# Optimization experiments

Measured on AMD Instinct MI355X. Metric: run time of the kernel, lower is better.

Reference implementation:

```python
import jax, jax.numpy as jnp
import numpy as np

NEG_SLOPE = 0.2
N_NODES = 50000
N_EDGES = 800000
IN_DIM = 256
HID_DIM = 256
HEADS = 8
HEAD_DIM = HID_DIM // HEADS


def setup_inputs() -> dict:
    key = jax.random.key(0)
    ks = jax.random.split(key, 12)
    def glorot(k, shape):
        fan = sum(shape[-2:]) if len(shape) > 1 else shape[-1] + 1
        return jax.random.normal(k, shape, jnp.float32) * jnp.sqrt(2.0 / fan)
    return {
        "data": jax.random.normal(ks[0], (N_NODES, IN_DIM), jnp.float32),
        "src": jax.random.randint(ks[1], (N_EDGES,), 0, N_NODES),
        "dst": jax.random.randint(ks[2], (N_EDGES,), 0, N_NODES),
        "W1": glorot(ks[3], (IN_DIM, HID_DIM)),
        "al1": glorot(ks[4], (HEADS, HEAD_DIM)),
        "ar1": glorot(ks[5], (HEADS, HEAD_DIM)),
        "b1": jnp.zeros((HID_DIM,), jnp.float32),
        "W2": glorot(ks[6], (HID_DIM, HID_DIM)),
        "al2": glorot(ks[7], (HEADS, HEAD_DIM)),
        "ar2": glorot(ks[8], (HEADS, HEAD_DIM)),
        "b2": jnp.zeros((HID_DIM,), jnp.float32),
    }


def gat_layer(x, src, dst, W, al, ar, b):
    """One DGL-style GATConv layer with ReLU activation."""
    N = x.shape[0]
    feat = (x @ W).reshape(N, HEADS, HEAD_DIM)            # [N,H,D]
    el = jnp.sum(feat * al[None], axis=-1)                # [N,H]
    er = jnp.sum(feat * ar[None], axis=-1)                # [N,H]
    e = el[src] + er[dst]                                  # [E,H]
    e = jnp.where(e > 0, e, NEG_SLOPE * e)                 # LeakyReLU(0.2)
    # segment softmax over incoming edges of each dst node
    m = jax.ops.segment_max(e, dst, num_segments=N)        # [N,H] (-inf for empty)
    a = jnp.exp(e - m[dst])                                # [E,H]
    denom = jax.ops.segment_sum(a, dst, num_segments=N)    # [N,H]
    alpha = a / denom[dst]                                 # [E,H]
    msg = feat[src] * alpha[:, :, None]                    # [E,H,D]
    out = jax.ops.segment_sum(msg, dst, num_segments=N)    # [N,H,D]
    out = out + b.reshape(1, HEADS, HEAD_DIM)
    out = jax.nn.relu(out)
    return out.reshape(N, HID_DIM)


def reference(data, src, dst, W1, al1, ar1, b1, W2, al2, ar2, b2):
    h = gat_layer(data, src, dst, W1, al1, ar1, b1)
    h = gat_layer(h, src, dst, W2, al2, ar2, b2)
    return h
```

## Files before the change

### kernel.cpp

```cpp
#include <hip/hip_runtime.h>

#define N_NODES 50000
#define N_EDGES 800000
#define DIM 256
#define HEADS 8
#define NEG_SLOPE 0.2f
#define MAXDEG 64
#define OVFCAP 65536

typedef unsigned short u16;
typedef float floatx4 __attribute__((ext_vector_type(4)));
typedef __bf16 bf16x8 __attribute__((ext_vector_type(8)));

__device__ __forceinline__ float b2f(u16 u) {
    union { unsigned int i; float f; } v; v.i = ((unsigned int)u) << 16; return v.f;
}
__device__ __forceinline__ u16 f2b(float f) {
    union { float f; unsigned int i; } v; v.f = f;
    unsigned int x = v.i;
    if ((x & 0x7f800000u) == 0x7f800000u && (x & 0x007fffffu)) {
        return (u16)((x >> 16) | 0x0040u);
    }
    unsigned int r = (x + 0x7fffu + ((x >> 16) & 1u)) >> 16;
    return (u16)r;
}

__global__ __launch_bounds__(256) void fill_u32(unsigned int* __restrict__ p,
                                                unsigned int v, int n) {
    int i = blockIdx.x * 256 + threadIdx.x;
    if (i < n) p[i] = v;
}

__global__ __launch_bounds__(256) void init_kernel(const unsigned int* __restrict__ d,
                                                   int* __restrict__ counts,
                                                   int* __restrict__ flag,
                                                   int* __restrict__ novf) {
    int i = blockIdx.x * 256 + threadIdx.x;
    if (i < N_NODES) counts[i] = 0;
    if (blockIdx.x == 0) {
        __shared__ int cnt;
        if (threadIdx.x == 0) { cnt = 0; *novf = 0; }
        __syncthreads();
        unsigned int w = d[threadIdx.x];
        int bad = 0;
        #pragma unroll
        for (int half = 0; half < 2; ++half) {
            u16 u = (u16)(w >> (16 * half));
            unsigned int e = (u >> 7) & 0xFFu;
            if (u != 0 && (e >= 141u || e <= 27u)) bad = 1;
        }
        atomicAdd(&cnt, bad);
        __syncthreads();
        if (threadIdx.x == 0) *flag = (cnt > 64) ? 1 : 0;
    }
}

__global__ __launch_bounds__(256) void prep_kernel(const void* __restrict__ W1,
                                                   const void* __restrict__ W2,
                                                   u16* __restrict__ Wt1,
                                                   u16* __restrict__ Wt2,
                                                   const int* __restrict__ flagp) {
    const int isf = *flagp;
    int b = blockIdx.x;
    const void* W = (b < 16) ? W1 : W2;
    u16* Wt = (b < 16) ? Wt1 : Wt2;
    int t = b & 15;
    int k0 = (t >> 2) * 64, n0 = (t & 3) * 64;
    __shared__ float lt[64][65];
    int c = threadIdx.x & 63, r0 = threadIdx.x >> 6;
    #pragma unroll
    for (int j = 0; j < 16; ++j) {
        int r = j * 4 + r0;
        lt[r][c] = isf ? ((const float*)W)[(k0 + r) * 256 + n0 + c]
                       : b2f(((const u16*)W)[(k0 + r) * 256 + n0 + c]);
    }
    __syncthreads();
    #pragma unroll
    for (int j = 0; j < 16; ++j) {
        int rn = j * 4 + r0;
        Wt[(n0 + rn) * 256 + k0 + c] = f2b(lt[c][rn]);
    }
}

__global__ __launch_bounds__(256) void build_kernel(const int* __restrict__ src,
                                                    const int* __restrict__ dst,
                                                    int* __restrict__ counts,
                                                    int* __restrict__ padded,
                                                    int* __restrict__ novf,
                                                    int2* __restrict__ ovf, int E) {
    int i = blockIdx.x * 256 + threadIdx.x;
    if (i < E) {
        int d = dst[i];
        int s = src[i];
        int pos = atomicAdd(&counts[d], 1);
        if (pos < MAXDEG) {
            padded[d * MAXDEG + pos] = s;
        } else {
            int oi = atomicAdd(novf, 1);
            if (oi < OVFCAP) { int2 pr; pr.x = d; pr.y = s; ovf[oi] = pr; }
        }
    }
}

__global__ __launch_bounds__(256) void hist_kernel(const int* __restrict__ dst,
                                                   int* __restrict__ counts, int E) {
    int i = blockIdx.x * 256 + threadIdx.x;
    if (i < E) atomicAdd(&counts[dst[i]], 1);
}

__global__ __launch_bounds__(256) void scan_partial(const int* __restrict__ counts,
                                                    int* __restrict__ partial, int n) {
    int b = blockIdx.x, tid = threadIdx.x;
    int base = b * 1024 + tid * 4;
    int s = 0;
    #pragma unroll
    for (int k = 0; k < 4; ++k) if (base + k < n) s += counts[base + k];
    int lane = tid & 63;
    #pragma unroll
    for (int off = 32; off; off >>= 1) s += __shfl_xor(s, off);
    __shared__ int wsum[4];
    if (lane == 0) wsum[tid >> 6] = s;
    __syncthreads();
    if (tid == 0) partial[b] = wsum[0] + wsum[1] + wsum[2] + wsum[3];
}

__global__ __launch_bounds__(64) void scan_offsets(const int* __restrict__ partial,
                                                   int* __restrict__ offsets,
                                                   int* __restrict__ row_ptr,
                                                   int nb, int n) {
    int t = threadIdx.x;
    int v0 = (t < nb) ? partial[t] : 0;
    int v = v0;
    #pragma unroll
    for (int d = 1; d < 64; d <<= 1) {
        int u = __shfl_up(v, d);
        if (t >= d) v += u;
    }
    if (t < nb) offsets[t] = v - v0;
    if (t == 63) row_ptr[n] = v;
}

__global__ __launch_bounds__(256) void scan_write(const int* __restrict__ counts,
                                                  const int* __restrict__ offsets,
                                                  int* __restrict__ row_ptr,
                                                  int* __restrict__ wptr, int n) {
    int b = blockIdx.x, tid = threadIdx.x;
    int base = b * 1024 + tid * 4;
    int v[4]; int s = 0;
    #pragma unroll
    for (int k = 0; k < 4; ++k) { v[k] = (base + k < n) ? counts[base + k] : 0; s += v[k]; }
    int lane = tid & 63, w = tid >> 6;
    int incl = s;
    #pragma unroll
    for (int d = 1; d < 64; d <<= 1) {
        int u = __shfl_up(incl, d);
        if (lane >= d) incl += u;
    }
    __shared__ int wsum[4];
    if (lane == 63) wsum[w] = incl;
    __syncthreads();
    int woff = 0;
    for (int i = 0; i < w; ++i) woff += wsum[i];
    int run = offsets[b] + woff + incl - s;
    #pragma unroll
    for (int k = 0; k < 4; ++k) {
        if (base + k < n) { row_ptr[base + k] = run; wptr[base + k] = run; run += v[k]; }
    }
}

__global__ __launch_bounds__(256) void scatter_kernel(const int* __restrict__ src,
                                                      const int* __restrict__ dst,
                                                      int* __restrict__ wptr,
                                                      int* __restrict__ src_sorted, int E) {
    int i = blockIdx.x * 256 + threadIdx.x;
    if (i < E) {
        int pos = atomicAdd(&wptr[dst[i]], 1);
        src_sorted[pos] = src[i];
    }
}

#define LDA 264

__global__ __launch_bounds__(256, 3) void gemm_fused(const void* __restrict__ Araw,
                                                     int maybe_f32,
                                                     const u16* __restrict__ Wt,
                                                     u16* __restrict__ outF,
                                                     float* __restrict__ el,
                                                     float* __restrict__ er,
                                                     const void* __restrict__ al,
                                                     const void* __restrict__ ar,
                                                     int M, const int* __restrict__ flagp) {
    const int isf = *flagp;
    const bool af32 = (maybe_f32 != 0) && (isf != 0);
    __shared__ u16 As[64][LDA];
    const int tid  = threadIdx.x;
    const int w    = tid >> 6;
    const int lane = tid & 63;
    const int quad = lane >> 4;
    const int l16  = lane & 15;
    const int m0   = blockIdx.x * 64;

    const u16* wbase = Wt + (size_t)(64 * w + l16) * 256 + quad * 8;

    bf16x8 bCur[4], bNxt[4], aCur[4], aNxt[4];
    #pragma unroll
    for (int t = 0; t < 4; ++t)
        bCur[t] = *(const bf16x8*)(wbase + (size_t)t * 16 * 256);

    if (af32) {
        const float* Af = (const float*)Araw;
        #pragma unroll
        for (int it = 0; it < 8; ++it) {
            int idx = it * 256 + tid;
            int r = idx >> 5;
            int c = (idx & 31) << 3;
            int gr = m0 + r;
            u16 tb[8];
            if (gr < M) {
                float4 f0 = *(const float4*)(Af + (size_t)gr * 256 + c);
                float4 f1 = *(const float4*)(Af + (size_t)gr * 256 + c + 4);
                tb[0] = f2b(f0.x); tb[1] = f2b(f0.y); tb[2] = f2b(f0.z); tb[3] = f2b(f0.w);
                tb[4] = f2b(f1.x); tb[5] = f2b(f1.y); tb[6] = f2b(f1.z); tb[7] = f2b(f1.w);
            } else {
                #pragma unroll
                for (int k = 0; k < 8; ++k) tb[k] = 0;
            }
            *(uint4*)&As[r][c] = *(uint4*)tb;
        }
    } else {
        const u16* Ab = (const u16*)Araw;
        #pragma unroll
        for (int it = 0; it < 8; ++it) {
            int idx = it * 256 + tid;
            int r = idx >> 5;
            int c = (idx & 31) << 3;
            int gr = m0 + r;
            if (gr < M) {
                *(uint4*)&As[r][c] = *(const uint4*)(Ab + (size_t)gr * 256 + c);
            } else {
                uint4 z = {0u, 0u, 0u, 0u};
                *(uint4*)&As[r][c] = z;
            }
        }
    }
    __syncthreads();

    #pragma unroll
    for (int i = 0; i < 4; ++i)
        aCur[i] = *(const bf16x8*)&As[16 * i + l16][quad * 8];

    floatx4 acc[4][4] = {};

    #pragma unroll
    for (int s = 0; s < 8; ++s) {
        if (s < 7) {
            #pragma unroll
            for (int t = 0; t < 4; ++t)
                bNxt[t] = *(const bf16x8*)(wbase + (size_t)t * 16 * 256 + (s + 1) * 32);
            #pragma unroll
            for (int i = 0; i < 4; ++i)
                aNxt[i] = *(const bf16x8*)&As[16 * i + l16][(s + 1) * 32 + quad * 8];
        }
        #pragma unroll
        for (int i = 0; i < 4; ++i)
            #pragma unroll
            for (int t = 0; t < 4; ++t)
                acc[i][t] = __builtin_amdgcn_mfma_f32_16x16x32_bf16(aCur[i], bCur[t], acc[i][t], 0, 0, 0);
        if (s < 7) {
            #pragma unroll
            for (int t = 0; t < 4; ++t) bCur[t] = bNxt[t];
            #pragma unroll
            for (int i = 0; i < 4; ++i) aCur[i] = aNxt[i];
        }
    }

    __syncthreads();
    u16* Ct = (u16*)As;
    #pragma unroll
    for (int i = 0; i < 4; ++i)
        #pragma unroll
        for (int t = 0; t < 4; ++t) {
            int col = 64 * w + 16 * t + l16;
            #pragma unroll
            for (int r = 0; r < 4; ++r)
                Ct[(16 * i + quad * 4 + r) * LDA + col] = f2b(acc[i][t][r]);
        }
    __syncthreads();
    #pragma unroll
    for (int it = 0; it < 4; ++it) {
        int idx = it * 256 + tid;
        int row = idx >> 4;
        int c16 = (idx & 15) * 16;
        int gr = m0 + row;
        if (gr < M) {
            uint4 v0 = *(const uint4*)&Ct[row * LDA + c16];
            uint4 v1 = *(const uint4*)&Ct[row * LDA + c16 + 8];
            *(uint4*)(outF + (size_t)gr * 256 + c16) = v0;
            *(uint4*)(outF + (size_t)gr * 256 + c16 + 8) = v1;
        }
    }

    float alv[4], arv[4];
    #pragma unroll
    for (int t = 0; t < 4; ++t) {
        int c = 64 * w + 16 * t + l16;
        alv[t] = isf ? ((const float*)al)[c] : b2f(((const u16*)al)[c]);
        arv[t] = isf ? ((const float*)ar)[c] : b2f(((const u16*)ar)[c]);
    }
    #pragma unroll
    for (int i = 0; i < 4; ++i)
        #pragma unroll
        for (int r = 0; r < 4; ++r) {
            int row = m0 + 16 * i + quad * 4 + r;
            #pragma unroll
            for (int tt = 0; tt < 2; ++tt) {
                float pl = acc[i][2 * tt][r] * alv[2 * tt] + acc[i][2 * tt + 1][r] * alv[2 * tt + 1];
                float pr = acc[i][2 * tt][r] * arv[2 * tt] + acc[i][2 * tt + 1][r] * arv[2 * tt + 1];
                #pragma unroll
                for (int mask = 1; mask <= 8; mask <<= 1) {
                    pl += __shfl_xor(pl, mask);
                    pr += __shfl_xor(pr, mask);
                }
                if (l16 == 0 && row < M) {
                    el[row * 8 + 2 * w + tt] = pl;
                    er[row * 8 + 2 * w + tt] = pr;
                }
            }
        }
}

__global__ __launch_bounds__(256) void aggregate_kernel(const u16* __restrict__ feat,
                                                        const float* __restrict__ el,
                                                        const float* __restrict__ er,
                                                        const void* __restrict__ bias,
                                                        const int* __restrict__ idxinfo,
                                                        const int* __restrict__ srcbuf,
                                                        void* __restrict__ out,
                                                        int out_mode,
                                                        int node0,
                                                        const int* __restrict__ flagp,
                                                        int pmode,
                                                        const int* __restrict__ novfp,
                                                        const int2* __restrict__ ovf) {
    const int isf = *flagp;
    const int lane = threadIdx.x & 63;
    const int node = node0 + blockIdx.x * 4 + (threadIdx.x >> 6);
    if (node >= N_NODES) return;
    const int h = lane >> 3;
    const int j = lane & 7;
    int beg, deg;
    if (pmode) { beg = node * MAXDEG; deg = idxinfo[node]; }
    else       { beg = idxinfo[node]; deg = idxinfo[node + 1] - beg; }
    const int dcap = (pmode && deg > MAXDEG) ? MAXDEG : deg;
    int nov = 0;
    if (pmode && deg > MAXDEG) { nov = *novfp; if (nov > OVFCAP) nov = OVFCAP; }
    const float ern = er[node * HEADS + h];

    float m0v = -1e30f, ss0 = 0.f;
    float m1v = -1e30f, ss1 = 0.f;
    for (int i = j; i < dcap; i += 16) {
        int s0 = srcbuf[beg + i];
        int i2 = i + 8;
        int s1 = (i2 < dcap) ? srcbuf[beg + i2] : 0;
        float e0 = el[s0 * 8 + h] + ern;
        float e1 = el[s1 * 8 + h] + ern;
        e0 = e0 > 0.f ? e0 : NEG_SLOPE * e0;
        e1 = e1 > 0.f ? e1 : NEG_SLOPE * e1;
        if (i2 >= dcap) e1 = -3e30f;
        float mn0 = fmaxf(m0v, e0);
        ss0 = ss0 * __expf(m0v - mn0) + __expf(e0 - mn0);
        m0v = mn0;
        float mn1 = fmaxf(m1v, e1);
        ss1 = ss1 * __expf(m1v - mn1) + __expf(e1 - mn1);
        m1v = mn1;
    }
    for (int k = j; k < nov; k += 8) {
        int2 pr = ovf[k];
        if (pr.x != node) continue;
        float e = el[pr.y * 8 + h] + ern;
        e = e > 0.f ? e : NEG_SLOPE * e;
        float mn = fmaxf(m0v, e);
        ss0 = ss0 * __expf(m0v - mn) + __expf(e - mn);
        m0v = mn;
    }
    float m = fmaxf(m0v, m1v);
    float ssum = ss0 * __expf(m0v - m) + ss1 * __expf(m1v - m);
    #pragma unroll
    for (int mask = 1; mask <= 4; mask <<= 1) {
        float mo = __shfl_xor(m, mask);
        float so = __shfl_xor(ssum, mask);
        float mn = fmaxf(m, mo);
        ssum = ssum * __expf(m - mn) + so * __expf(mo - mn);
        m = mn;
    }
    const float mx = m;
    const float inv = ssum > 0.f ? 1.f / ssum : 0.f;

    const int q = lane & 31;
    const int half = lane >> 5;
    const int hq = q >> 2;
    float a[8] = {};

    int sC = 0; float avC = 0.f;
    if (j < dcap) {
        sC = srcbuf[beg + j];
        float e = el[sC * 8 + h] + ern;
        e = e > 0.f ? e : NEG_SLOPE * e;
        avC = __expf(e - mx) * inv;
    }
    uint4 f[4]; float ae[4];
    #pragma unroll
    for (int u = 0; u < 4; ++u) {
        int sel = hq * 8 + 2 * u + half;
        int se = __shfl(sC, sel);
        ae[u] = __shfl(avC, sel);
        f[u] = *(const uint4*)(feat + (size_t)se * DIM + 8 * q);
    }

    #pragma unroll 2
    for (int c0 = 0; c0 < dcap; c0 += 8) {
        uint4 f2[4]; float ae2[4];
        {
            int sN = 0; float avN = 0.f;
            int i = c0 + 8 + j;
            if (i < dcap) {
                sN = srcbuf[beg + i];
                float e = el[sN * 8 + h] + ern;
                e = e > 0.f ? e : NEG_SLOPE * e;
                avN = __expf(e - mx) * inv;
            }
            #pragma unroll
            for (int u = 0; u < 4; ++u) {
                int sel = hq * 8 + 2 * u + half;
                int se = __shfl(sN, sel);
                ae2[u] = __shfl(avN, sel);
                f2[u] = *(const uint4*)(feat + (size_t)se * DIM + 8 * q);
            }
        }
        #pragma unroll
        for (int u = 0; u < 4; ++u) {
            float wgt = ae[u];
            a[0] += wgt * b2f((u16)(f[u].x & 0xffffu)); a[1] += wgt * b2f((u16)(f[u].x >> 16));
            a[2] += wgt * b2f((u16)(f[u].y & 0xffffu)); a[3] += wgt * b2f((u16)(f[u].y >> 16));
            a[4] += wgt * b2f((u16)(f[u].z & 0xffffu)); a[5] += wgt * b2f((u16)(f[u].z >> 16));
            a[6] += wgt * b2f((u16)(f[u].w & 0xffffu)); a[7] += wgt * b2f((u16)(f[u].w >> 16));
        }
        #pragma unroll
        for (int u = 0; u < 4; ++u) { f[u] = f2[u]; ae[u] = ae2[u]; }
    }

    if (nov) {
        const float mxq  = __shfl(mx, hq * 8);
        const float invq = __shfl(inv, hq * 8);
        const float ernq = __shfl(ern, hq * 8);
        for (int k = 0; k < nov; ++k) {
            int2 pr = ovf[k];
            if (pr.x != node) continue;
            float av = 0.f;
            if (half == 0) {
                float e = el[pr.y * 8 + hq] + ernq;
                e = e > 0.f ? e : NEG_SLOPE * e;
                av = __expf(e - mxq) * invq;
            }
            uint4 fv = *(const uint4*)(feat + (size_t)pr.y * DIM + 8 * q);
            a[0] += av * b2f((u16)(fv.x & 0xffffu)); a[1] += av * b2f((u16)(fv.x >> 16));
            a[2] += av * b2f((u16)(fv.y & 0xffffu)); a[3] += av * b2f((u16)(fv.y >> 16));
            a[4] += av * b2f((u16)(fv.z & 0xffffu)); a[5] += av * b2f((u16)(fv.z >> 16));
            a[6] += av * b2f((u16)(fv.w & 0xffffu)); a[7] += av * b2f((u16)(fv.w >> 16));
        }
    }

    #pragma unroll
    for (int k = 0; k < 8; ++k) a[k] += __shfl_xor(a[k], 32);

    if (half == 0) {
        float o[8];
        if (isf) {
            float4 b0 = *(const float4*)((const float*)bias + 8 * q);
            float4 b1 = *(const float4*)((const float*)bias + 8 * q + 4);
            o[0] = a[0] + b0.x; o[1] = a[1] + b0.y; o[2] = a[2] + b0.z; o[3] = a[3] + b0.w;
            o[4] = a[4] + b1.x; o[5] = a[5] + b1.y; o[6] = a[6] + b1.z; o[7] = a[7] + b1.w;
        } else {
            uint4 bu = *(const uint4*)((const u16*)bias + 8 * q);
            o[0] = a[0] + b2f((u16)(bu.x & 0xffffu)); o[1] = a[1] + b2f((u16)(bu.x >> 16));
            o[2] = a[2] + b2f((u16)(bu.y & 0xffffu)); o[3] = a[3] + b2f((u16)(bu.y >> 16));
            o[4] = a[4] + b2f((u16)(bu.z & 0xffffu)); o[5] = a[5] + b2f((u16)(bu.z >> 16));
            o[6] = a[6] + b2f((u16)(bu.w & 0xffffu)); o[7] = a[7] + b2f((u16)(bu.w >> 16));
        }
        #pragma unroll
        for (int k = 0; k < 8; ++k) o[k] = fmaxf(o[k], 0.f);
        if (out_mode == 0 || !isf) {
            u16 pk[8] = {f2b(o[0]), f2b(o[1]), f2b(o[2]), f2b(o[3]),
                         f2b(o[4]), f2b(o[5]), f2b(o[6]), f2b(o[7])};
            *(uint4*)((u16*)out + (size_t)node * DIM + 8 * q) = *(uint4*)pk;
        } else {
            float4 v0 = {o[0], o[1], o[2], o[3]};
            float4 v1 = {o[4], o[5], o[6], o[7]};
            *(float4*)((float*)out + (size_t)node * DIM + 8 * q) = v0;
            *(float4*)((float*)out + (size_t)node * DIM + 8 * q + 4) = v1;
        }
    }
}

extern "C" void kernel_launch(void* const* d_in, const int* in_sizes, int n_in,
                              void* d_out, int out_size, void* d_ws, size_t ws_size,
                              hipStream_t stream) {
    const void* data = d_in[0];
    const int* src = (const int*)d_in[1];
    const int* dst = (const int*)d_in[2];
    const void* W1  = d_in[3];
    const void* al1 = d_in[4];
    const void* ar1 = d_in[5];
    const void* b1  = d_in[6];
    const void* W2  = d_in[7];
    const void* al2 = d_in[8];
    const void* ar2 = d_in[9];
    const void* b2  = d_in[10];

    const size_t BASE =
        (size_t)N_NODES * DIM * 2 +
        (size_t)N_NODES * HEADS * 4 * 2 +
        (size_t)N_NODES * 4 +
        2 * 256 * 256 * 2 +
        1024;
    const size_t NEEDED_PAD = BASE + (size_t)N_NODES * MAXDEG * 4 + (size_t)OVFCAP * 8;
    const size_t NEEDED_CSR = BASE + (size_t)N_NODES * 4 +
                              (size_t)(N_NODES + 4) * 4 +
                              (size_t)N_EDGES * 4;

    if (ws_size < NEEDED_CSR && ws_size < NEEDED_PAD) {
        int nwords = (out_size + 1) / 2;
        fill_u32<<<(nwords + 255) / 256, 256, 0, stream>>>(
            (unsigned int*)d_out, 0x42C842C8u, nwords);
        return;
    }

    char* ws = (char*)d_ws;
    u16* feat = (u16*)ws;        ws += (size_t)N_NODES * DIM * 2;
    float* el = (float*)ws;      ws += (size_t)N_NODES * HEADS * 4;
    float* er = (float*)ws;      ws += (size_t)N_NODES * HEADS * 4;
    int* counts = (int*)ws;      ws += (size_t)N_NODES * 4;
    u16* Wt1 = (u16*)ws;         ws += 256 * 256 * 2;
    u16* Wt2 = (u16*)ws;         ws += 256 * 256 * 2;
    int* flag = (int*)ws;        ws += 256;
    int* novf = (int*)ws;        ws += 256;
    int* partial = (int*)ws;     ws += 256;
    int* offsets = (int*)ws;     ws += 256;

    u16* h1 = (u16*)d_out;
    const int gemm_blocks = (N_NODES + 63) / 64;
    const int HALF = 25000;
    const int agg_half_blocks = HALF / 4;

    init_kernel<<<(N_NODES + 255) / 256, 256, 0, stream>>>(
        (const unsigned int*)data, counts, flag, novf);
    prep_kernel<<<32, 256, 0, stream>>>(W1, W2, Wt1, Wt2, flag);

    const int* idxinfo;
    const int* srcbuf;
    const int2* ovf = (const int2*)d_ws;
    int pmode;

    if (ws_size >= NEEDED_PAD) {
        int* padded = (int*)ws;  ws += (size_t)N_NODES * MAXDEG * 4;
        int2* ovfw = (int2*)ws;  ws += (size_t)OVFCAP * 8;
        build_kernel<<<(N_EDGES + 255) / 256, 256, 0, stream>>>(
            src, dst, counts, padded, novf, ovfw, N_EDGES);
        idxinfo = counts; srcbuf = padded; ovf = ovfw; pmode = 1;
    } else {
        int* wptr = (int*)ws;        ws += (size_t)N_NODES * 4;
        int* row_ptr = (int*)ws;     ws += (size_t)(N_NODES + 4) * 4;
        int* src_sorted = (int*)ws;  ws += (size_t)N_EDGES * 4;
        const int nb = (N_NODES + 1023) / 1024;
        hist_kernel<<<(N_EDGES + 255) / 256, 256, 0, stream>>>(dst, counts, N_EDGES);
        scan_partial<<<nb, 256, 0, stream>>>(counts, partial, N_NODES);
        scan_offsets<<<1, 64, 0, stream>>>(partial, offsets, row_ptr, nb, N_NODES);
        scan_write<<<nb, 256, 0, stream>>>(counts, offsets, row_ptr, wptr, N_NODES);
        scatter_kernel<<<(N_EDGES + 255) / 256, 256, 0, stream>>>(src, dst, wptr, src_sorted, N_EDGES);
        idxinfo = row_ptr; srcbuf = src_sorted; pmode = 0;
    }

    gemm_fused<<<gemm_blocks, 256, 0, stream>>>(data, 1, Wt1, feat,
                                                el, er, al1, ar1, N_NODES, flag);
    aggregate_kernel<<<agg_half_blocks, 256, 0, stream>>>(feat, el, er, b1, idxinfo, srcbuf,
                                                          (void*)h1, 0, 0, flag, pmode, novf, ovf);
    aggregate_kernel<<<agg_half_blocks, 256, 0, stream>>>(feat, el, er, b1, idxinfo, srcbuf,
                                                          (void*)h1, 0, HALF, flag, pmode, novf, ovf);
    gemm_fused<<<gemm_blocks, 256, 0, stream>>>(h1, 0, Wt2, feat,
                                                el, er, al2, ar2, N_NODES, flag);
    aggregate_kernel<<<agg_half_blocks, 256, 0, stream>>>(feat, el, er, b2, idxinfo, srcbuf,
                                                          d_out, 2, 0, flag, pmode, novf, ovf);
    aggregate_kernel<<<agg_half_blocks, 256, 0, stream>>>(feat, el, er, b2, idxinfo, srcbuf,
                                                          d_out, 2, HALF, flag, pmode, novf, ovf);
}
```

Before: 394.4 us.

## Fuse edge-list build into first GEMM launch and shrink GEMM tile to 32 rows

Merges the padded adjacency build kernel with the first-layer GEMM into one launch, interleaving build blocks and GEMM blocks 1:2 so the atomic-heavy build overlaps the MFMA work. The GEMM drops the LDS staging of A and of the output: A fragments are loaded straight from global into registers, and results are written directly to global memory. The tile is halved to 32 rows with occupancy 4. This removes a launch and the LDS traffic, but adds uncoalesced 2-byte output stores and redundant A loads across the four waves.

```diff
diff --git a/kernel.cpp b/kernel.cpp
--- a/kernel.cpp
+++ b/kernel.cpp
@@ -82,26 +82,6 @@
     }
 }
 
-__global__ __launch_bounds__(256) void build_kernel(const int* __restrict__ src,
-                                                    const int* __restrict__ dst,
-                                                    int* __restrict__ counts,
-                                                    int* __restrict__ padded,
-                                                    int* __restrict__ novf,
-                                                    int2* __restrict__ ovf, int E) {
-    int i = blockIdx.x * 256 + threadIdx.x;
-    if (i < E) {
-        int d = dst[i];
-        int s = src[i];
-        int pos = atomicAdd(&counts[d], 1);
-        if (pos < MAXDEG) {
-            padded[d * MAXDEG + pos] = s;
-        } else {
-            int oi = atomicAdd(novf, 1);
-            if (oi < OVFCAP) { int2 pr; pr.x = d; pr.y = s; ovf[oi] = pr; }
-        }
-    }
-}
-
 __global__ __launch_bounds__(256) void hist_kernel(const int* __restrict__ dst,
                                                    int* __restrict__ counts, int E) {
     int i = blockIdx.x * 256 + threadIdx.x;
@@ -179,126 +159,86 @@
     }
 }
 
-#define LDA 264
-
-__global__ __launch_bounds__(256, 3) void gemm_fused(const void* __restrict__ Araw,
-                                                     int maybe_f32,
-                                                     const u16* __restrict__ Wt,
-                                                     u16* __restrict__ outF,
-                                                     float* __restrict__ el,
-                                                     float* __restrict__ er,
-                                                     const void* __restrict__ al,
-                                                     const void* __restrict__ ar,
-                                                     int M, const int* __restrict__ flagp) {
-    const int isf = *flagp;
+__device__ __forceinline__ void gemm_body(int gid, const void* __restrict__ Araw,
+                                          int maybe_f32,
+                                          const u16* __restrict__ Wt,
+                                          u16* __restrict__ outF,
+                                          float* __restrict__ el,
+                                          float* __restrict__ er,
+                                          const void* __restrict__ al,
+                                          const void* __restrict__ ar,
+                                          int M, int isf) {
     const bool af32 = (maybe_f32 != 0) && (isf != 0);
-    __shared__ u16 As[64][LDA];
     const int tid  = threadIdx.x;
     const int w    = tid >> 6;
     const int lane = tid & 63;
     const int quad = lane >> 4;
     const int l16  = lane & 15;
-    const int m0   = blockIdx.x * 64;
+    const int m0   = gid * 32;
 
     const u16* wbase = Wt + (size_t)(64 * w + l16) * 256 + quad * 8;
-
-    bf16x8 bCur[4], bNxt[4], aCur[4], aNxt[4];
-    #pragma unroll
-    for (int t = 0; t < 4; ++t)
-        bCur[t] = *(const bf16x8*)(wbase + (size_t)t * 16 * 256);
-
-    if (af32) {
-        const float* Af = (const float*)Araw;
+    const float* Af = (const float*)Araw;
+    const u16* Ab = (const u16*)Araw;
+    const int rbase = m0 + l16;
+
+    u16 zb[8] = {};
+    const bf16x8 ZERO = *(const bf16x8*)zb;
+
+    bf16x8 aC[2], aN[2], bC[4], bN[4];
+    floatx4 acc[2][4] = {};
+
+#define LOADB(s, dstb) { \
+    _Pragma("unroll") \
+    for (int t = 0; t < 4; ++t) \
+        dstb[t] = *(const bf16x8*)(wbase + (size_t)t * 16 * 256 + (s) * 32); }
+
+#define LOADA(s, dsta) { \
+    _Pragma("unroll") \
+    for (int i = 0; i < 2; ++i) { \
+        int row_ = rbase + 16 * i; \
+        if (row_ < M) { \
+            if (af32) { \
+                const float* p_ = Af + (size_t)row_ * 256 + (s) * 32 + quad * 8; \
+                float4 f0_ = *(const float4*)p_; \
+                float4 f1_ = *(const float4*)(p_ + 4); \
+                u16 tb_[8] = {f2b(f0_.x), f2b(f0_.y), f2b(f0_.z), f2b(f0_.w), \
+                              f2b(f1_.x), f2b(f1_.y), f2b(f1_.z), f2b(f1_.w)}; \
+                dsta[i] = *(const bf16x8*)tb_; \
+            } else { \
+                dsta[i] = *(const bf16x8*)(Ab + (size_t)row_ * 256 + (s) * 32 + quad * 8); \
+            } \
+        } else dsta[i] = ZERO; } }
+
+    LOADB(0, bC);
+    LOADA(0, aC);
+
+    #pragma unroll
+    for (int s = 0; s < 8; ++s) {
+        if (s < 7) { LOADB(s + 1, bN); LOADA(s + 1, aN); }
         #pragma unroll
-        for (int it = 0; it < 8; ++it) {
-            int idx = it * 256 + tid;
-            int r = idx >> 5;
-            int c = (idx & 31) << 3;
-            int gr = m0 + r;
-            u16 tb[8];
-            if (gr < M) {
-                float4 f0 = *(const float4*)(Af + (size_t)gr * 256 + c);
-                float4 f1 = *(const float4*)(Af + (size_t)gr * 256 + c + 4);
-                tb[0] = f2b(f0.x); tb[1] = f2b(f0.y); tb[2] = f2b(f0.z); tb[3] = f2b(f0.w);
-                tb[4] = f2b(f1.x); tb[5] = f2b(f1.y); tb[6] = f2b(f1.z); tb[7] = f2b(f1.w);
-            } else {
-                #pragma unroll
-                for (int k = 0; k < 8; ++k) tb[k] = 0;
-            }
-            *(uint4*)&As[r][c] = *(uint4*)tb;
-        }
-    } else {
-        const u16* Ab = (const u16*)Araw;
-        #pragma unroll
-        for (int it = 0; it < 8; ++it) {
-            int idx = it * 256 + tid;
-            int r = idx >> 5;
-            int c = (idx & 31) << 3;
-            int gr = m0 + r;
-            if (gr < M) {
-                *(uint4*)&As[r][c] = *(const uint4*)(Ab + (size_t)gr * 256 + c);
-            } else {
-                uint4 z = {0u, 0u, 0u, 0u};
-                *(uint4*)&As[r][c] = z;
-            }
-        }
-    }
-    __syncthreads();
-
-    #pragma unroll
-    for (int i = 0; i < 4; ++i)
-        aCur[i] = *(const bf16x8*)&As[16 * i + l16][quad * 8];
-
-    floatx4 acc[4][4] = {};
-
-    #pragma unroll
-    for (int s = 0; s < 8; ++s) {
+        for (int i = 0; i < 2; ++i)
+            #pragma unroll
+            for (int t = 0; t < 4; ++t)
+                acc[i][t] = __builtin_amdgcn_mfma_f32_16x16x32_bf16(aC[i], bC[t], acc[i][t], 0, 0, 0);
         if (s < 7) {
             #pragma unroll
-            for (int t = 0; t < 4; ++t)
-                bNxt[t] = *(const bf16x8*)(wbase + (size_t)t * 16 * 256 + (s + 1) * 32);
+            for (int t = 0; t < 4; ++t) bC[t] = bN[t];
             #pragma unroll
-            for (int i = 0; i < 4; ++i)
-                aNxt[i] = *(const bf16x8*)&As[16 * i + l16][(s + 1) * 32 + quad * 8];
-        }
+            for (int i = 0; i < 2; ++i) aC[i] = aN[i];
+        }
+    }
+#undef LOADA
+#undef LOADB
+
+    #pragma unroll
+    for (int i = 0; i < 2; ++i)
         #pragma unroll
-        for (int i = 0; i < 4; ++i)
+        for (int t = 0; t < 4; ++t)
             #pragma unroll
-            for (int t = 0; t < 4; ++t)
-                acc[i][t] = __builtin_amdgcn_mfma_f32_16x16x32_bf16(aCur[i], bCur[t], acc[i][t], 0, 0, 0);
-        if (s < 7) {
-            #pragma unroll
-            for (int t = 0; t < 4; ++t) bCur[t] = bNxt[t];
-            #pragma unroll
-            for (int i = 0; i < 4; ++i) aCur[i] = aNxt[i];
-        }
-    }
-
-    __syncthreads();
-    u16* Ct = (u16*)As;
-    #pragma unroll
-    for (int i = 0; i < 4; ++i)
-        #pragma unroll
-        for (int t = 0; t < 4; ++t) {
-            int col = 64 * w + 16 * t + l16;
-            #pragma unroll
-            for (int r = 0; r < 4; ++r)
-                Ct[(16 * i + quad * 4 + r) * LDA + col] = f2b(acc[i][t][r]);
-        }
-    __syncthreads();
-    #pragma unroll
-    for (int it = 0; it < 4; ++it) {
-        int idx = it * 256 + tid;
-        int row = idx >> 4;
-        int c16 = (idx & 15) * 16;
-        int gr = m0 + row;
-        if (gr < M) {
-            uint4 v0 = *(const uint4*)&Ct[row * LDA + c16];
-            uint4 v1 = *(const uint4*)&Ct[row * LDA + c16 + 8];
-            *(uint4*)(outF + (size_t)gr * 256 + c16) = v0;
-            *(uint4*)(outF + (size_t)gr * 256 + c16 + 8) = v1;
-        }
-    }
+            for (int r = 0; r < 4; ++r) {
+                int row = m0 + 16 * i + quad * 4 + r;
+                if (row < M) outF[(size_t)row * 256 + 64 * w + 16 * t + l16] = f2b(acc[i][t][r]);
+            }
 
     float alv[4], arv[4];
     #pragma unroll
@@ -308,7 +248,7 @@
         arv[t] = isf ? ((const float*)ar)[c] : b2f(((const u16*)ar)[c]);
     }
     #pragma unroll
-    for (int i = 0; i < 4; ++i)
+    for (int i = 0; i < 2; ++i)
         #pragma unroll
         for (int r = 0; r < 4; ++r) {
             int row = m0 + 16 * i + quad * 4 + r;
@@ -327,6 +267,71 @@
                 }
             }
         }
+}
+
+__global__ __launch_bounds__(256, 4) void gemm_kernel(const void* __restrict__ Araw,
+                                                      int maybe_f32,
+                                                      const u16* __restrict__ Wt,
+                                                      u16* __restrict__ outF,
+                                                      float* __restrict__ el,
+                                                      float* __restrict__ er,
+                                                      const void* __restrict__ al,
+                                                      const void* __restrict__ ar,
+                                                      int M, const int* __restrict__ flagp) {
+    gemm_body(blockIdx.x, Araw, maybe_f32, Wt, outF, el, er, al, ar, M, *flagp);
+}
+
+__global__ __launch_bounds__(256, 4) void gemm_build_kernel(const void* __restrict__ Araw,
+                                                            int maybe_f32,
+                                                            const u16* __restrict__ Wt,
+                                                            u16* __restrict__ outF,
+                                                            float* __restrict__ el,
+                                                            float* __restrict__ er,
+                                                            const void* __restrict__ al,
+                                                            const void* __restrict__ ar,
+                                                            int M, const int* __restrict__ flagp,
+                                                            const int* __restrict__ src,
+                                                            const int* __restrict__ dst,
+                                                            int* __restrict__ counts,
+                                                            int* __restrict__ padded,
+                                                            int* __restrict__ novf,
+                                                            int2* __restrict__ ovf,
+                                                            int E, int GB) {
+    const int bx = blockIdx.x;
+    const int r3 = bx % 3;
+    if (r3 == 2) {
+        int base = (bx / 3) * 1024 + threadIdx.x * 4;
+        if (base + 3 < E) {
+            int4 d4 = *(const int4*)(dst + base);
+            int4 s4 = *(const int4*)(src + base);
+            int p0 = atomicAdd(&counts[d4.x], 1);
+            int p1 = atomicAdd(&counts[d4.y], 1);
+            int p2 = atomicAdd(&counts[d4.z], 1);
+            int p3 = atomicAdd(&counts[d4.w], 1);
+            if (p0 < MAXDEG) padded[d4.x * MAXDEG + p0] = s4.x;
+            else { int oi = atomicAdd(novf, 1); if (oi < OVFCAP) { int2 pr; pr.x = d4.x; pr.y = s4.x; ovf[oi] = pr; } }
+            if (p1 < MAXDEG) padded[d4.y * MAXDEG + p1] = s4.y;
+            else { int oi = atomicAdd(novf, 1); if (oi < OVFCAP) { int2 pr; pr.x = d4.y; pr.y = s4.y; ovf[oi] = pr; } }
+            if (p2 < MAXDEG) padded[d4.z * MAXDEG + p2] = s4.z;
+            else { int oi = atomicAdd(novf, 1); if (oi < OVFCAP) { int2 pr; pr.x = d4.z; pr.y = s4.z; ovf[oi] = pr; } }
+            if (p3 < MAXDEG) padded[d4.w * MAXDEG + p3] = s4.w;
+            else { int oi = atomicAdd(novf, 1); if (oi < OVFCAP) { int2 pr; pr.x = d4.w; pr.y = s4.w; ovf[oi] = pr; } }
+        } else {
+            for (int k = 0; k < 4; ++k) {
+                int i = base + k;
+                if (i < E) {
+                    int d = dst[i], s = src[i];
+                    int pos = atomicAdd(&counts[d], 1);
+                    if (pos < MAXDEG) padded[d * MAXDEG + pos] = s;
+                    else { int oi = atomicAdd(novf, 1); if (oi < OVFCAP) { int2 pr; pr.x = d; pr.y = s; ovf[oi] = pr; } }
+                }
+            }
+        }
+    } else {
+        int gid = (bx / 3) * 2 + r3;
+        if (gid < GB)
+            gemm_body(gid, Araw, maybe_f32, Wt, outF, el, er, al, ar, M, *flagp);
+    }
 }
 
 __global__ __launch_bounds__(256) void aggregate_kernel(const u16* __restrict__ feat,
@@ -548,7 +553,7 @@
     int* offsets = (int*)ws;     ws += 256;
 
     u16* h1 = (u16*)d_out;
-    const int gemm_blocks = (N_NODES + 63) / 64;
+    const int GB = (N_NODES + 31) / 32;
     const int HALF = 25000;
     const int agg_half_blocks = HALF / 4;
 
@@ -564,8 +569,11 @@
     if (ws_size >= NEEDED_PAD) {
         int* padded = (int*)ws;  ws += (size_t)N_NODES * MAXDEG * 4;
         int2* ovfw = (int2*)ws;  ws += (size_t)OVFCAP * 8;
-        build_kernel<<<(N_EDGES + 255) / 256, 256, 0, stream>>>(
-            src, dst, counts, padded, novf, ovfw, N_EDGES);
+        const int build_blocks = (N_EDGES + 1023) / 1024;
+        const int fused_blocks = 3 * build_blocks;
+        gemm_build_kernel<<<fused_blocks, 256, 0, stream>>>(
+            data, 1, Wt1, feat, el, er, al1, ar1, N_NODES, flag,
+            src, dst, counts, padded, novf, ovfw, N_EDGES, GB);
         idxinfo = counts; srcbuf = padded; ovf = ovfw; pmode = 1;
     } else {
         int* wptr = (int*)ws;        ws += (size_t)N_NODES * 4;
@@ -578,16 +586,16 @@
         scan_write<<<nb, 256, 0, stream>>>(counts, offsets, row_ptr, wptr, N_NODES);
         scatter_kernel<<<(N_EDGES + 255) / 256, 256, 0, stream>>>(src, dst, wptr, src_sorted, N_EDGES);
         idxinfo = row_ptr; srcbuf = src_sorted; pmode = 0;
-    }
-
-    gemm_fused<<<gemm_blocks, 256, 0, stream>>>(data, 1, Wt1, feat,
-                                                el, er, al1, ar1, N_NODES, flag);
+        gemm_kernel<<<GB, 256, 0, stream>>>(data, 1, Wt1, feat,
+                                            el, er, al1, ar1, N_NODES, flag);
+    }
+
     aggregate_kernel<<<agg_half_blocks, 256, 0, stream>>>(feat, el, er, b1, idxinfo, srcbuf,
                                                           (void*)h1, 0, 0, flag, pmode, novf, ovf);
     aggregate_kernel<<<agg_half_blocks, 256, 0, stream>>>(feat, el, er, b1, idxinfo, srcbuf,
                                                           (void*)h1, 0, HALF, flag, pmode, novf, ovf);
-    gemm_fused<<<gemm_blocks, 256, 0, stream>>>(h1, 0, Wt2, feat,
-                                                el, er, al2, ar2, N_NODES, flag);
+    gemm_kernel<<<GB, 256, 0, stream>>>(h1, 0, Wt2, feat,
+                                        el, er, al2, ar2, N_NODES, flag);
     aggregate_kernel<<<agg_half_blocks, 256, 0, stream>>>(feat, el, er, b2, idxinfo, srcbuf,
                                                           d_out, 2, 0, flag, pmode, novf, ovf);
     aggregate_kernel<<<agg_half_blocks, 256, 0, stream>>>(feat, el, er, b2, idxinfo, srcbuf,
```

Result: slower. 414.7 us (+5.1%).
